# Kernel tuning notes

Hardware: AMD Instinct MI355X
Metric: run time of the kernel (lower is better)

Reference implementation:

```python
import jax, jax.numpy as jnp
import numpy as np

N_VOX = 150000
GRID = 256
C_IN = 32
C_OUT = 64
EPS = 1e-5


def _build_neighbor_idx(n=N_VOX, g=GRID, seed=0):
    # Build a submanifold-conv rulebook: for each of 27 kernel offsets and each
    # output voxel, the index of the input voxel at that offset, or -1 if absent.
    rng = np.random.default_rng(seed)
    lin = rng.choice(g ** 3, size=n, replace=False).astype(np.int64)
    coords = np.stack(np.unravel_index(lin, (g, g, g)), axis=1)  # [N,3]
    order = np.argsort(lin)
    sorted_keys = lin[order]
    offs = np.array([[dx, dy, dz] for dx in (-1, 0, 1) for dy in (-1, 0, 1) for dz in (-1, 0, 1)], dtype=np.int64)  # [27,3]
    nbr = np.full((27, n), -1, dtype=np.int32)
    for k in range(27):
        nc = coords + offs[k]  # neighbor coords [N,3]
        valid = np.all((nc >= 0) & (nc < g), axis=1)
        nkey = (nc[:, 0] * g + nc[:, 1]) * g + nc[:, 2]
        pos = np.searchsorted(sorted_keys, nkey)
        pos_c = np.clip(pos, 0, n - 1)
        found = valid & (sorted_keys[pos_c] == nkey)
        nbr[k] = np.where(found, order[pos_c].astype(np.int32), -1)
    return jnp.asarray(nbr)


def setup_inputs() -> dict:
    key = jax.random.key(0)
    k1, k2, k3, k4 = jax.random.split(key, 4)
    features = jax.random.normal(k1, (N_VOX, C_IN), dtype=jnp.float32)
    weight = jax.random.normal(k2, (27, C_IN, C_OUT), dtype=jnp.float32) * 0.05
    gamma = jax.random.uniform(k3, (C_OUT,), dtype=jnp.float32, minval=0.5, maxval=1.5)
    beta = jax.random.normal(k4, (C_OUT,), dtype=jnp.float32) * 0.1
    neighbor_idx = _build_neighbor_idx()
    return {"features": features, "weight": weight, "gamma": gamma, "beta": beta, "neighbor_idx": neighbor_idx}


def reference(features, weight, gamma, beta, neighbor_idx):
    # --- SubMConv3d via rulebook gather -> GEMM -> (implicit) scatter ---
    safe_idx = jnp.maximum(neighbor_idx, 0)            # [K,N]
    gathered = features[safe_idx]                      # [K,N,Cin]
    mask = (neighbor_idx >= 0)[..., None]              # [K,N,1]
    gathered = jnp.where(mask, gathered, jnp.zeros((), features.dtype))
    out = jnp.einsum('knc,kcd->nd', gathered, weight)  # [N,Cout]
    # --- BatchNorm1d (training-mode batch stats, biased var) + ReLU ---
    mean = jnp.mean(out, axis=0)
    var = jnp.mean(jnp.square(out - mean), axis=0)
    normed = (out - mean) * jax.lax.rsqrt(var + EPS)
    return jax.nn.relu(normed * gamma + beta)
```

## Files before the change

kernel.cpp:

```cpp
#include <hip/hip_runtime.h>

#define NV    150000
#define CIN   32
#define COUT  64
#define EPSF  1e-5f
#define NCOPY 16

#define NTHR   256
#define NTILES (NV / 16)
#define NBLK1  ((NTILES + 3) / 4)

#define CH8    (NV * COUT / 8)
#define NBLK2  1172
#define STRIDE2 (NBLK2 * NTHR)

#define FEAT_T   (NV * CIN / 8)
#define FEATBLK  ((FEAT_T + NTHR - 1) / NTHR)
#define PREPBLK  (FEATBLK + 27 + 1)

#define WS_WFRAG  9600000
#define WS_GSTATS 9710592
#define WS_OUTBF  9720832

typedef short  bf16x8 __attribute__((ext_vector_type(8)));
typedef float  f32x4  __attribute__((ext_vector_type(4)));

union u4bf { uint4 u; bf16x8 h; };

__device__ __forceinline__ unsigned pack_bf2(float a, float b) {
    union { float f; unsigned u; } ca, cb;
    ca.f = a; cb.f = b;
    const unsigned lo = (ca.u + 0x7FFFu + ((ca.u >> 16) & 1u)) >> 16;
    const unsigned hi = (cb.u + 0x7FFFu + ((cb.u >> 16) & 1u)) & 0xFFFF0000u;
    return lo | hi;
}

__device__ __forceinline__ unsigned short bf16r(float a) {
    union { float f; unsigned u; } c; c.f = a;
    return (unsigned short)((c.u + 0x7FFFu + ((c.u >> 16) & 1u)) >> 16);
}

__global__ __launch_bounds__(NTHR) void k_prep(
    const float* __restrict__ feat,
    const float* __restrict__ weight,
    char*        __restrict__ ws)
{
    const int b = blockIdx.x;
    if (b < FEATBLK) {
        const int t = b * NTHR + threadIdx.x;
        if (t < FEAT_T) {
            const float4* src = (const float4*)(feat) + t * 2;
            const float4 f0 = src[0];
            const float4 f1 = src[1];
            uint4 o;
            o.x = pack_bf2(f0.x, f0.y);
            o.y = pack_bf2(f0.z, f0.w);
            o.z = pack_bf2(f1.x, f1.y);
            o.w = pack_bf2(f1.z, f1.w);
            ((uint4*)ws)[t] = o;
        }
    } else if (b < FEATBLK + 27) {
        const int k    = b - FEATBLK;
        const int bb   = threadIdx.x >> 6;
        const int lane = threadIdx.x & 63;
        const int quad = lane >> 4;
        const int lm   = lane & 15;
        const float* wsrc = weight + (long)k * CIN * COUT + (quad * 8) * COUT + bb * 16 + lm;
        float f[8];
#pragma unroll
        for (int j = 0; j < 8; ++j) f[j] = wsrc[j * COUT];
        uint4 o;
        o.x = pack_bf2(f[0], f[1]);
        o.y = pack_bf2(f[2], f[3]);
        o.z = pack_bf2(f[4], f[5]);
        o.w = pack_bf2(f[6], f[7]);
        ((uint4*)(ws + WS_WFRAG))[(k * 4 + bb) * 64 + lane] = o;
    } else {
        float* gs = (float*)(ws + WS_GSTATS);
#pragma unroll
        for (int i = 0; i < 8; ++i) gs[threadIdx.x + i * NTHR] = 0.f;
    }
}

__global__ __launch_bounds__(NTHR) void k_conv(
    char*        __restrict__ ws,
    const int*   __restrict__ nbr,
    float*       __restrict__ gstats)
{
    const uint4* fb = (const uint4*)ws;
    const uint4* wf = (const uint4*)(ws + WS_WFRAG);
    unsigned short* ob = (unsigned short*)(ws + WS_OUTBF);

    const int tid  = threadIdx.x;
    const int lane = tid & 63;
    const int quad = lane >> 4;
    const int lm   = lane & 15;
    const int wid  = blockIdx.x * 4 + (tid >> 6);

    f32x4 ssum = {0.f, 0.f, 0.f, 0.f};
    f32x4 qsum = {0.f, 0.f, 0.f, 0.f};
    f32x4 acc[4] = {{0.f,0.f,0.f,0.f},{0.f,0.f,0.f,0.f},{0.f,0.f,0.f,0.f},{0.f,0.f,0.f,0.f}};

    const bool have_tile = (wid < NTILES);
    const int v0 = have_tile ? wid * 16 : 0;

    if (have_tile) {
        int sidx[7];
#pragma unroll
        for (int it = 0; it < 7; ++it) {
            const int item = lane + it * 64;
            int idx = -1;
            if (item < 416) {
                const int kp = item >> 4;
                const int k  = kp + (kp >= 13);
                idx = nbr[(long)k * NV + v0 + (item & 15)];
            }
            sidx[it] = idx;
        }

        {
            u4bf a; a.u = fb[(v0 + lm) * 4 + quad];
#pragma unroll
            for (int b = 0; b < 4; ++b) {
                u4bf w; w.u = wf[(13 * 4 + b) * 64 + lane];
                acc[b] = __builtin_amdgcn_mfma_f32_16x16x32_bf16(a.h, w.h, acc[b], 0, 0, 0);
            }
        }

        unsigned int kmask = 0u;
#pragma unroll
        for (int it = 0; it < 7; ++it) {
            const unsigned long long m = __ballot(sidx[it] >= 0);
            kmask |= ((m & 0xFFFFull)         ? 1u : 0u) << (it * 4 + 0);
            kmask |= (((m >> 16) & 0xFFFFull) ? 1u : 0u) << (it * 4 + 1);
            kmask |= (((m >> 32) & 0xFFFFull) ? 1u : 0u) << (it * 4 + 2);
            kmask |= ((m >> 48)               ? 1u : 0u) << (it * 4 + 3);
        }

        while (kmask) {
            const int kpA = __ffs(kmask) - 1;
            kmask &= kmask - 1u;
            int kpB = -1;
            if (kmask) { kpB = __ffs(kmask) - 1; kmask &= kmask - 1u; }
            const int kA = kpA + (kpA >= 13);
            const int kB = (kpB >= 0) ? (kpB + (kpB >= 13)) : kA;

            int rawA, rawB;
            switch (kpA >> 2) {
                case 0: rawA = sidx[0]; break; case 1: rawA = sidx[1]; break;
                case 2: rawA = sidx[2]; break; case 3: rawA = sidx[3]; break;
                case 4: rawA = sidx[4]; break; case 5: rawA = sidx[5]; break;
                default: rawA = sidx[6]; break;
            }
            const int kpB2 = (kpB >= 0) ? kpB : kpA;
            switch (kpB2 >> 2) {
                case 0: rawB = sidx[0]; break; case 1: rawB = sidx[1]; break;
                case 2: rawB = sidx[2]; break; case 3: rawB = sidx[3]; break;
                case 4: rawB = sidx[4]; break; case 5: rawB = sidx[5]; break;
                default: rawB = sidx[6]; break;
            }
            const int idxA = __shfl(rawA, ((kpA & 3) << 4) | lm);
            int idxB = __shfl(rawB, ((kpB2 & 3) << 4) | lm);
            if (kpB < 0) idxB = -1;

            u4bf aA, aB;
            aA.u = fb[(long)(idxA < 0 ? 0 : idxA) * 4 + quad];
            aB.u = fb[(long)(idxB < 0 ? 0 : idxB) * 4 + quad];
            if (idxA < 0) aA.u = make_uint4(0u, 0u, 0u, 0u);
            if (idxB < 0) aB.u = make_uint4(0u, 0u, 0u, 0u);

#pragma unroll
            for (int b = 0; b < 4; ++b) {
                u4bf wA, wB;
                wA.u = wf[(kA * 4 + b) * 64 + lane];
                wB.u = wf[(kB * 4 + b) * 64 + lane];
                acc[b] = __builtin_amdgcn_mfma_f32_16x16x32_bf16(aA.h, wA.h, acc[b], 0, 0, 0);
                acc[b] = __builtin_amdgcn_mfma_f32_16x16x32_bf16(aB.h, wB.h, acc[b], 0, 0, 0);
            }
        }

#pragma unroll
        for (int b = 0; b < 4; ++b) {
            const float r0 = acc[b][0], r1 = acc[b][1], r2 = acc[b][2], r3 = acc[b][3];
            ob[(long)(v0 + quad * 4 + 0) * COUT + b * 16 + lm] = bf16r(r0);
            ob[(long)(v0 + quad * 4 + 1) * COUT + b * 16 + lm] = bf16r(r1);
            ob[(long)(v0 + quad * 4 + 2) * COUT + b * 16 + lm] = bf16r(r2);
            ob[(long)(v0 + quad * 4 + 3) * COUT + b * 16 + lm] = bf16r(r3);
            ssum[b] += r0 + r1 + r2 + r3;
            qsum[b] += r0 * r0 + r1 * r1 + r2 * r2 + r3 * r3;
        }
    }

#pragma unroll
    for (int off = 16; off < 64; off <<= 1) {
#pragma unroll
        for (int b = 0; b < 4; ++b) {
            ssum[b] += __shfl_xor(ssum[b], off);
            qsum[b] += __shfl_xor(qsum[b], off);
        }
    }

    __shared__ float ls[4][128];
    const int wv = tid >> 6;
    if (quad == 0) {
#pragma unroll
        for (int b = 0; b < 4; ++b) {
            ls[wv][b * 16 + lm]      = ssum[b];
            ls[wv][64 + b * 16 + lm] = qsum[b];
        }
    }
    __syncthreads();
    if (tid < 128) {
        const float v = ls[0][tid] + ls[1][tid] + ls[2][tid] + ls[3][tid];
        atomicAdd(gstats + (blockIdx.x & (NCOPY - 1)) * 128 + tid, v);
    }
}

__global__ __launch_bounds__(NTHR) void k_norm(
    const char*  __restrict__ ws_ro,
    float*       __restrict__ out,
    const float* __restrict__ gstats,
    const float* __restrict__ gamma,
    const float* __restrict__ beta)
{
    __shared__ float sscale[COUT];
    __shared__ float sshift[COUT];
    const int tid = threadIdx.x;
    if (tid < COUT) {
        float s = 0.f, q = 0.f;
#pragma unroll
        for (int cp = 0; cp < NCOPY; ++cp) {
            s += gstats[cp * 128 + tid];
            q += gstats[cp * 128 + 64 + tid];
        }
        const float inv_n = 1.f / (float)NV;
        const float mean = s * inv_n;
        float var = q * inv_n - mean * mean;
        var = fmaxf(var, 0.f);
        const float rstd = rsqrtf(var + EPSF);
        const float sc = gamma[tid] * rstd;
        sscale[tid] = sc;
        sshift[tid] = beta[tid] - mean * sc;
    }
    __syncthreads();

    const int  base = blockIdx.x * NTHR + tid;
    const int  g8   = (base & 7) * 8;
    const float4 SC0 = make_float4(sscale[g8],   sscale[g8+1], sscale[g8+2], sscale[g8+3]);
    const float4 SC1 = make_float4(sscale[g8+4], sscale[g8+5], sscale[g8+6], sscale[g8+7]);
    const float4 SH0 = make_float4(sshift[g8],   sshift[g8+1], sshift[g8+2], sshift[g8+3]);
    const float4 SH1 = make_float4(sshift[g8+4], sshift[g8+5], sshift[g8+6], sshift[g8+7]);

    const uint4* ib = (const uint4*)(ws_ro + WS_OUTBF);
    float4* o4 = (float4*)out;

#pragma unroll
    for (int n = 0; n < 4; ++n) {
        const int c = base + n * STRIDE2;
        if (n == 3 && c >= CH8) break;
        const uint4 u = ib[c];
        union { unsigned u; float f; } t;
        float4 v0, v1;
        t.u = u.x << 16;          v0.x = t.f;
        t.u = u.x & 0xFFFF0000u;  v0.y = t.f;
        t.u = u.y << 16;          v0.z = t.f;
        t.u = u.y & 0xFFFF0000u;  v0.w = t.f;
        t.u = u.z << 16;          v1.x = t.f;
        t.u = u.z & 0xFFFF0000u;  v1.y = t.f;
        t.u = u.w << 16;          v1.z = t.f;
        t.u = u.w & 0xFFFF0000u;  v1.w = t.f;

        v0.x = fmaxf(v0.x * SC0.x + SH0.x, 0.f);
        v0.y = fmaxf(v0.y * SC0.y + SH0.y, 0.f);
        v0.z = fmaxf(v0.z * SC0.z + SH0.z, 0.f);
        v0.w = fmaxf(v0.w * SC0.w + SH0.w, 0.f);
        v1.x = fmaxf(v1.x * SC1.x + SH1.x, 0.f);
        v1.y = fmaxf(v1.y * SC1.y + SH1.y, 0.f);
        v1.z = fmaxf(v1.z * SC1.z + SH1.z, 0.f);
        v1.w = fmaxf(v1.w * SC1.w + SH1.w, 0.f);

        o4[(long)c * 2]     = v0;
        o4[(long)c * 2 + 1] = v1;
    }
}

extern "C" void kernel_launch(void* const* d_in, const int* in_sizes, int n_in,
                              void* d_out, int out_size, void* d_ws, size_t ws_size,
                              hipStream_t stream) {
    const float* feat   = (const float*)d_in[0];
    const float* weight = (const float*)d_in[1];
    const float* gamma  = (const float*)d_in[2];
    const float* beta   = (const float*)d_in[3];
    const int*   nbr    = (const int*)d_in[4];
    float* out = (float*)d_out;

    char*  ws     = (char*)d_ws;
    float* gstats = (float*)(ws + WS_GSTATS);

    k_prep<<<PREPBLK, NTHR, 0, stream>>>(feat, weight, ws);
    k_conv<<<NBLK1, NTHR, 0, stream>>>(ws, nbr, gstats);
    k_norm<<<NBLK2, NTHR, 0, stream>>>(ws, out, gstats, gamma, beta);
}
```

Measured before the change: 116.1 us.

## Process two voxel tiles per wave with shared center weights and prefetched indices

```diff
diff --git a/kernel.cpp b/kernel.cpp
--- a/kernel.cpp
+++ b/kernel.cpp
@@ -8,7 +8,7 @@
 
 #define NTHR   256
 #define NTILES (NV / 16)
-#define NBLK1  ((NTILES + 3) / 4)
+#define NBLK1  1172
 
 #define CH8    (NV * COUT / 8)
 #define NBLK2  1172
@@ -99,38 +99,54 @@
 
     f32x4 ssum = {0.f, 0.f, 0.f, 0.f};
     f32x4 qsum = {0.f, 0.f, 0.f, 0.f};
-    f32x4 acc[4] = {{0.f,0.f,0.f,0.f},{0.f,0.f,0.f,0.f},{0.f,0.f,0.f,0.f},{0.f,0.f,0.f,0.f}};
-
-    const bool have_tile = (wid < NTILES);
-    const int v0 = have_tile ? wid * 16 : 0;
-
-    if (have_tile) {
-        int sidx[7];
+
+    const int t0 = wid * 2;
+    const int t1 = wid * 2 + 1;
+    const bool have0 = (t0 < NTILES);
+    const bool have1 = (t1 < NTILES);
+    const int v0a = have0 ? t0 * 16 : 0;
+    const int v0b = have1 ? t1 * 16 : 0;
+
+    int sidx[2][7];
+#pragma unroll
+    for (int it = 0; it < 7; ++it) {
+        const int item = lane + it * 64;
+        int idxA = -1, idxB = -1;
+        if (item < 416) {
+            const int kp = item >> 4;
+            const int k  = kp + (kp >= 13);
+            const long base = (long)k * NV + (item & 15);
+            idxA = have0 ? nbr[base + v0a] : -1;
+            idxB = have1 ? nbr[base + v0b] : -1;
+        }
+        sidx[0][it] = idxA;
+        sidx[1][it] = idxB;
+    }
+
+    u4bf a0, a1, wc[4];
+    a0.u = fb[(v0a + lm) * 4 + quad];
+    a1.u = fb[(v0b + lm) * 4 + quad];
+#pragma unroll
+    for (int b = 0; b < 4; ++b) wc[b].u = wf[(13 * 4 + b) * 64 + lane];
+
+#pragma unroll 1
+    for (int t = 0; t < 2; ++t) {
+        const bool have = t ? have1 : have0;
+        if (!have) break;
+        const int v0 = t ? v0b : v0a;
+
+        f32x4 acc[4] = {{0.f,0.f,0.f,0.f},{0.f,0.f,0.f,0.f},{0.f,0.f,0.f,0.f},{0.f,0.f,0.f,0.f}};
+        {
+            const u4bf a = t ? a1 : a0;
+#pragma unroll
+            for (int b = 0; b < 4; ++b)
+                acc[b] = __builtin_amdgcn_mfma_f32_16x16x32_bf16(a.h, wc[b].h, acc[b], 0, 0, 0);
+        }
+
+        unsigned int kmask = 0u;
 #pragma unroll
         for (int it = 0; it < 7; ++it) {
-            const int item = lane + it * 64;
-            int idx = -1;
-            if (item < 416) {
-                const int kp = item >> 4;
-                const int k  = kp + (kp >= 13);
-                idx = nbr[(long)k * NV + v0 + (item & 15)];
-            }
-            sidx[it] = idx;
-        }
-
-        {
-            u4bf a; a.u = fb[(v0 + lm) * 4 + quad];
-#pragma unroll
-            for (int b = 0; b < 4; ++b) {
-                u4bf w; w.u = wf[(13 * 4 + b) * 64 + lane];
-                acc[b] = __builtin_amdgcn_mfma_f32_16x16x32_bf16(a.h, w.h, acc[b], 0, 0, 0);
-            }
-        }
-
-        unsigned int kmask = 0u;
-#pragma unroll
-        for (int it = 0; it < 7; ++it) {
-            const unsigned long long m = __ballot(sidx[it] >= 0);
+            const unsigned long long m = __ballot(sidx[t][it] >= 0);
             kmask |= ((m & 0xFFFFull)         ? 1u : 0u) << (it * 4 + 0);
             kmask |= (((m >> 16) & 0xFFFFull) ? 1u : 0u) << (it * 4 + 1);
             kmask |= (((m >> 32) & 0xFFFFull) ? 1u : 0u) << (it * 4 + 2);
@@ -147,17 +163,17 @@
 
             int rawA, rawB;
             switch (kpA >> 2) {
-                case 0: rawA = sidx[0]; break; case 1: rawA = sidx[1]; break;
-                case 2: rawA = sidx[2]; break; case 3: rawA = sidx[3]; break;
-                case 4: rawA = sidx[4]; break; case 5: rawA = sidx[5]; break;
-                default: rawA = sidx[6]; break;
+                case 0: rawA = sidx[t][0]; break; case 1: rawA = sidx[t][1]; break;
+                case 2: rawA = sidx[t][2]; break; case 3: rawA = sidx[t][3]; break;
+                case 4: rawA = sidx[t][4]; break; case 5: rawA = sidx[t][5]; break;
+                default: rawA = sidx[t][6]; break;
             }
             const int kpB2 = (kpB >= 0) ? kpB : kpA;
             switch (kpB2 >> 2) {
-                case 0: rawB = sidx[0]; break; case 1: rawB = sidx[1]; break;
-                case 2: rawB = sidx[2]; break; case 3: rawB = sidx[3]; break;
-                case 4: rawB = sidx[4]; break; case 5: rawB = sidx[5]; break;
-                default: rawB = sidx[6]; break;
+                case 0: rawB = sidx[t][0]; break; case 1: rawB = sidx[t][1]; break;
+                case 2: rawB = sidx[t][2]; break; case 3: rawB = sidx[t][3]; break;
+                case 4: rawB = sidx[t][4]; break; case 5: rawB = sidx[t][5]; break;
+                default: rawB = sidx[t][6]; break;
             }
             const int idxA = __shfl(rawA, ((kpA & 3) << 4) | lm);
             int idxB = __shfl(rawB, ((kpB2 & 3) << 4) | lm);
```

New measurement: 130.0 us. 12.0% more time.
